# Performance work log

Hardware: AMD Instinct MI355X
Metric: run time of the kernel (lower is better)

Reference implementation:

```python
import jax, jax.numpy as jnp
import numpy as np

H = W = 256
C = 256
N_ROIS = 2000
POOL = 7


def setup_inputs() -> dict:
    key = jax.random.key(0)
    kf, kw, kh, kx, ky = jax.random.split(key, 5)
    feature_map = jax.random.normal(kf, (1, H, W, C), dtype=jnp.float32)
    # ROI format: (batch_idx, x, y, w, h), integer pixel coords, in-bounds
    w = jax.random.randint(kw, (N_ROIS,), 8, 65)
    h = jax.random.randint(kh, (N_ROIS,), 8, 65)
    x = jax.random.randint(kx, (N_ROIS,), 0, W - 64)
    y = jax.random.randint(ky, (N_ROIS,), 0, H - 64)
    rois = jnp.stack([jnp.zeros_like(x), x, y, w, h], axis=1).astype(jnp.int32)
    return {"feature_map": feature_map, "rois": rois, "pool_size": POOL}


def _axis_coords(start, length, pool_size):
    """Sample coords along one axis, matching tf.image.resize bilinear
    (half-pixel centers) applied to the crop [start, start+length).
    start, length: [N] int. Returns abs idx0, idx1 [N,P] int and frac [N,P]."""
    lf = length.astype(jnp.float32)
    # source coord within the crop for each output pixel
    f = (jnp.arange(pool_size, dtype=jnp.float32) + 0.5)[None, :] * (lf / pool_size)[:, None] - 0.5
    f = jnp.clip(f, 0.0, (lf - 1.0)[:, None])
    i0 = jnp.floor(f).astype(jnp.int32)
    i1 = jnp.minimum(i0 + 1, (length - 1)[:, None])
    frac = f - i0.astype(jnp.float32)
    return start[:, None] + i0, start[:, None] + i1, frac


def _roi_pool(feature_map, rois, pool_size):
    fm = feature_map[0]                      # [H, W, C]
    x, y, w, h = rois[:, 1], rois[:, 2], rois[:, 3], rois[:, 4]
    y0, y1, fy = _axis_coords(y, h, pool_size)   # [N, P]
    x0, x1, fx = _axis_coords(x, w, pool_size)   # [N, P]

    def g(yi, xi):  # gather -> [N, P, P, C]
        return fm[yi[:, :, None], xi[:, None, :], :]

    fx_ = fx[:, None, :, None]
    fy_ = fy[:, :, None, None]
    top = g(y0, x0) * (1.0 - fx_) + g(y0, x1) * fx_
    bot = g(y1, x0) * (1.0 - fx_) + g(y1, x1) * fx_
    return top * (1.0 - fy_) + bot * fy_     # [N, P, P, C]


def reference(feature_map, rois, pool_size):
    return _roi_pool(feature_map, rois, pool_size)
```

## Files before the change

kernel.cpp:

```cpp
#include <hip/hip_runtime.h>

#define FH 256
#define FW 256
#define FC 256
#define POOL 7

__global__ __launch_bounds__(256) void roi_pool_kernel(
    const float* __restrict__ fm,
    const int*   __restrict__ rois,
    float*       __restrict__ out,
    int n_rois)
{
    int t = blockIdx.x * blockDim.x + threadIdx.x;
    int total = n_rois * POOL * POOL * (FC / 4);
    if (t >= total) return;

    int lane = t & 63;
    int cell = t >> 6;
    int pi   = cell % POOL;
    int tmp  = cell / POOL;
    int pj   = tmp % POOL;
    int roi  = tmp / POOL;

    int rx = rois[roi * 5 + 1];
    int ry = rois[roi * 5 + 2];
    int rw = rois[roi * 5 + 3];
    int rh = rois[roi * 5 + 4];

    float lfh = (float)rh;
    float fy  = ((float)pj + 0.5f) * (lfh / (float)POOL) - 0.5f;
    fy = fminf(fmaxf(fy, 0.0f), lfh - 1.0f);
    int   j0 = (int)floorf(fy);
    int   j1 = min(j0 + 1, rh - 1);
    float wy = fy - (float)j0;
    int   y0 = ry + j0;
    int   y1 = ry + j1;

    float lfw = (float)rw;
    float fx  = ((float)pi + 0.5f) * (lfw / (float)POOL) - 0.5f;
    fx = fminf(fmaxf(fx, 0.0f), lfw - 1.0f);
    int   i0 = (int)floorf(fx);
    int   i1 = min(i0 + 1, rw - 1);
    float wx = fx - (float)i0;
    int   x0 = rx + i0;
    int   x1 = rx + i1;

    const float4* p00 = (const float4*)(fm + ((size_t)y0 * FW + x0) * FC) + lane;
    const float4* p01 = (const float4*)(fm + ((size_t)y0 * FW + x1) * FC) + lane;
    const float4* p10 = (const float4*)(fm + ((size_t)y1 * FW + x0) * FC) + lane;
    const float4* p11 = (const float4*)(fm + ((size_t)y1 * FW + x1) * FC) + lane;

    float4 a = *p00;
    float4 b = *p01;
    float4 c = *p10;
    float4 d = *p11;

    float owx = 1.0f - wx;
    float owy = 1.0f - wy;

    float4 r;
    {
        float top = a.x * owx + b.x * wx;
        float bot = c.x * owx + d.x * wx;
        r.x = top * owy + bot * wy;
    }
    {
        float top = a.y * owx + b.y * wx;
        float bot = c.y * owx + d.y * wx;
        r.y = top * owy + bot * wy;
    }
    {
        float top = a.z * owx + b.z * wx;
        float bot = c.z * owx + d.z * wx;
        r.z = top * owy + bot * wy;
    }
    {
        float top = a.w * owx + b.w * wx;
        float bot = c.w * owx + d.w * wx;
        r.w = top * owy + bot * wy;
    }

    float4* o = (float4*)(out + (size_t)cell * FC) + lane;
    *o = r;
}

extern "C" void kernel_launch(void* const* d_in, const int* in_sizes, int n_in,
                              void* d_out, int out_size, void* d_ws, size_t ws_size,
                              hipStream_t stream) {
    const float* fm   = (const float*)d_in[0];
    const int*   rois = (const int*)d_in[1];
    float* out = (float*)d_out;

    int n_rois = in_sizes[1] / 5;
    int total  = n_rois * POOL * POOL * (FC / 4);
    int block  = 256;
    int grid   = (total + block - 1) / block;

    roi_pool_kernel<<<grid, block, 0, stream>>>(fm, rois, out, n_rois);
}
```

Before: 181.0 us.

## Remap workgroups to XCD-contiguous chunks and use nontemporal output stores

Remaps blockIdx so each of the 8 XCDs processes a contiguous range of logical blocks, keeping neighbouring ROI cells on the same XCD and its L2 cache. Switches the output writes to nontemporal stores so the large write-only output does not evict feature-map lines from cache. The interpolation math is also rewritten with ext_vector_type, which is mostly cosmetic. The remap assumes round-robin dispatch of workgroups across XCDs.

```diff
diff --git a/kernel.cpp b/kernel.cpp
--- a/kernel.cpp
+++ b/kernel.cpp
@@ -5,13 +5,23 @@
 #define FC 256
 #define POOL 7
 
+typedef float f32x4 __attribute__((ext_vector_type(4)));
+
 __global__ __launch_bounds__(256) void roi_pool_kernel(
     const float* __restrict__ fm,
     const int*   __restrict__ rois,
     float*       __restrict__ out,
     int n_rois)
 {
-    int t = blockIdx.x * blockDim.x + threadIdx.x;
+    int nwg  = gridDim.x;
+    int q    = nwg >> 3;
+    int rr   = nwg & 7;
+    int xcd  = blockIdx.x & 7;
+    int slot = blockIdx.x >> 3;
+    int base = (xcd < rr) ? xcd * (q + 1) : rr * (q + 1) + (xcd - rr) * q;
+    int lb   = base + slot;
+
+    int t = lb * 256 + (int)threadIdx.x;
     int total = n_rois * POOL * POOL * (FC / 4);
     if (t >= total) return;
 
@@ -45,43 +55,25 @@
     int   x0 = rx + i0;
     int   x1 = rx + i1;
 
-    const float4* p00 = (const float4*)(fm + ((size_t)y0 * FW + x0) * FC) + lane;
-    const float4* p01 = (const float4*)(fm + ((size_t)y0 * FW + x1) * FC) + lane;
-    const float4* p10 = (const float4*)(fm + ((size_t)y1 * FW + x0) * FC) + lane;
-    const float4* p11 = (const float4*)(fm + ((size_t)y1 * FW + x1) * FC) + lane;
+    const f32x4* p00 = (const f32x4*)(fm + ((size_t)y0 * FW + x0) * FC) + lane;
+    const f32x4* p01 = (const f32x4*)(fm + ((size_t)y0 * FW + x1) * FC) + lane;
+    const f32x4* p10 = (const f32x4*)(fm + ((size_t)y1 * FW + x0) * FC) + lane;
+    const f32x4* p11 = (const f32x4*)(fm + ((size_t)y1 * FW + x1) * FC) + lane;
 
-    float4 a = *p00;
-    float4 b = *p01;
-    float4 c = *p10;
-    float4 d = *p11;
+    f32x4 a = *p00;
+    f32x4 b = *p01;
+    f32x4 c = *p10;
+    f32x4 d = *p11;
 
     float owx = 1.0f - wx;
     float owy = 1.0f - wy;
 
-    float4 r;
-    {
-        float top = a.x * owx + b.x * wx;
-        float bot = c.x * owx + d.x * wx;
-        r.x = top * owy + bot * wy;
-    }
-    {
-        float top = a.y * owx + b.y * wx;
-        float bot = c.y * owx + d.y * wx;
-        r.y = top * owy + bot * wy;
-    }
-    {
-        float top = a.z * owx + b.z * wx;
-        float bot = c.z * owx + d.z * wx;
-        r.z = top * owy + bot * wy;
-    }
-    {
-        float top = a.w * owx + b.w * wx;
-        float bot = c.w * owx + d.w * wx;
-        r.w = top * owy + bot * wy;
-    }
+    f32x4 top = a * owx + b * wx;
+    f32x4 bot = c * owx + d * wx;
+    f32x4 res = top * owy + bot * wy;
 
-    float4* o = (float4*)(out + (size_t)cell * FC) + lane;
-    *o = r;
+    f32x4* o = (f32x4*)(out + (size_t)cell * FC) + lane;
+    __builtin_nontemporal_store(res, o);
 }
 
 extern "C" void kernel_launch(void* const* d_in, const int* in_sizes, int n_in,
```

After: 182.3 us. About the same (+0.7%).
